# Optimization experiments

Measured on AMD Instinct MI355X. Metric: run time of the kernel, lower is better.

Reference implementation:

```python
import jax, jax.numpy as jnp
import numpy as np

WS = 7  # window size
NH = 12  # num heads
EPS = 1e-5


def setup_inputs() -> dict:
    key = jax.random.key(0)
    ks = jax.random.split(key, 12)
    B, H, W, C = 32, 56, 56, 384
    Dff = 4 * C
    s = lambda k, shape, scale=0.02: jax.random.normal(k, shape, dtype=jnp.float32) * scale
    return {
        "x": jax.random.normal(ks[0], (B, H, W, C), dtype=jnp.float32),
        "ln1_g": jnp.ones((C,), jnp.float32), "ln1_b": jnp.zeros((C,), jnp.float32),
        "qkv_w": s(ks[1], (C, 3 * C)), "qkv_b": jnp.zeros((3 * C,), jnp.float32),
        "proj_w": s(ks[2], (C, C)), "proj_b": jnp.zeros((C,), jnp.float32),
        "ln2_g": jnp.ones((C,), jnp.float32), "ln2_b": jnp.zeros((C,), jnp.float32),
        "mlp_w1": s(ks[3], (C, Dff)), "mlp_b1": jnp.zeros((Dff,), jnp.float32),
        "mlp_w2": s(ks[4], (Dff, C)), "mlp_b2": jnp.zeros((C,), jnp.float32),
    }


def _layernorm(x, g, b):
    m = jnp.mean(x, axis=-1, keepdims=True)
    v = jnp.mean(jnp.square(x - m), axis=-1, keepdims=True)
    return (x - m) * jax.lax.rsqrt(v + EPS) * g + b


def reference(x, ln1_g, ln1_b, qkv_w, qkv_b, proj_w, proj_b, ln2_g, ln2_b,
              mlp_w1, mlp_b1, mlp_w2, mlp_b2):
    B, H, W, C = x.shape
    N = WS * WS
    hd = C // NH
    shortcut = x
    xn = _layernorm(x, ln1_g, ln1_b)
    # window partition: [B,H,W,C] -> [B*nW, N, C]
    xw = xn.reshape(B, H // WS, WS, W // WS, WS, C).transpose(0, 1, 3, 2, 4, 5)
    xw = xw.reshape(-1, N, C)
    # attention within each 49-token window
    qkv = (xw @ qkv_w + qkv_b).reshape(-1, N, 3, NH, hd)
    qkv = qkv.transpose(2, 0, 3, 1, 4)  # [3, Bn, h, N, d]
    q, k, v = qkv[0] * (hd ** -0.5), qkv[1], qkv[2]
    attn = jax.nn.softmax(jnp.einsum('bhnd,bhmd->bhnm', q, k), axis=-1)
    out = jnp.einsum('bhnm,bhmd->bhnd', attn, v)  # [Bn, h, N, d]
    out = out.transpose(0, 2, 1, 3).reshape(-1, N, C)
    out = out @ proj_w + proj_b
    # window unpartition
    xa = out.reshape(B, H // WS, W // WS, WS, WS, C).transpose(0, 1, 3, 2, 4, 5)
    xa = xa.reshape(B, H, W, C)
    x = shortcut + xa
    # MLP (dropout inactive at inference); Keras gelu default is exact
    h = jax.nn.gelu(_layernorm(x, ln2_g, ln2_b) @ mlp_w1 + mlp_b1, approximate=False)
    return x + (h @ mlp_w2 + mlp_b2)
```

## Files before the change

kernel.cpp:

```cpp
#include <hip/hip_runtime.h>
#include <hip/hip_bf16.h>
#include <cstdint>

typedef __bf16 bf16;
typedef __bf16 bf16x8 __attribute__((ext_vector_type(8)));
typedef float f32x4 __attribute__((ext_vector_type(4)));
typedef unsigned int u32;
typedef unsigned short u16;

#define DEV static __device__ __forceinline__

DEV float bfbits2f(u32 bits) { return __builtin_bit_cast(float, bits << 16); }
DEV u16 f2bfbits(float f) {
  u32 u = __builtin_bit_cast(u32, f);
  u32 r = (u + 0x7fffu + ((u >> 16) & 1u)) >> 16;
  return (u16)r;
}

__global__ __launch_bounds__(256) void probe_k(const u32* __restrict__ x, u32* __restrict__ flag) {
  __shared__ int cnt[256];
  int t = threadIdx.x;
  int c = 0;
#pragma unroll
  for (int i = 0; i < 4; ++i) {
    u32 u = x[t * 4 + i];
    u32 e = (u >> 7) & 0xFF;
    c += (e >= 110 && e <= 140) ? 1 : 0;
  }
  cnt[t] = c;
  __syncthreads();
  for (int s = 128; s > 0; s >>= 1) {
    if (t < s) cnt[t] += cnt[t + s];
    __syncthreads();
  }
  if (t == 0) flag[0] = (cnt[0] > 512) ? 1u : 0u;
}

__global__ __launch_bounds__(256) void cvt_params_k(const void* p0, const void* p1,
                                                    const void* p2, const void* p3,
                                                    const void* p4, const void* p5,
                                                    const void* p6, const void* p7,
                                                    float* __restrict__ out,
                                                    const u32* __restrict__ flag) {
  int i = blockIdx.x * 256 + threadIdx.x;
  if (i >= 4992) return;
  const int bounds[9] = {0, 1152, 1536, 3072, 3456, 3840, 4224, 4608, 4992};
  const void* ps[8] = {p0, p1, p2, p3, p4, p5, p6, p7};
  int seg = 0;
  while (i >= bounds[seg + 1]) ++seg;
  int off = i - bounds[seg];
  bool isbf = flag[0] != 0;
  out[i] = isbf ? bfbits2f(((const u16*)ps[seg])[off]) : ((const float*)ps[seg])[off];
}

__global__ __launch_bounds__(256) void transpose_k(const void* __restrict__ in,
                                                   u16* __restrict__ out, int R, int Cc,
                                                   const u32* __restrict__ flag) {
  bool isbf = flag[0] != 0;
  __shared__ u16 tile[32][33];
  int bx = blockIdx.x * 32, by = blockIdx.y * 32;
  int tx = threadIdx.x & 31, ty = threadIdx.x >> 5;
#pragma unroll
  for (int i = 0; i < 32; i += 8) {
    size_t idx = (size_t)(by + ty + i) * Cc + bx + tx;
    u16 v = isbf ? ((const u16*)in)[idx] : f2bfbits(((const float*)in)[idx]);
    tile[ty + i][tx] = v;
  }
  __syncthreads();
#pragma unroll
  for (int i = 0; i < 32; i += 8)
    out[(size_t)(bx + ty + i) * R + by + tx] = tile[tx][ty + i];
}

template <int RAWSRC>
__global__ __launch_bounds__(256) void ln_kernel(const void* __restrict__ xv,
                                                 const float* __restrict__ g,
                                                 const float* __restrict__ b,
                                                 u32* __restrict__ out,
                                                 const u32* __restrict__ flag,
                                                 int windowed, int t0) {
  const int t = t0 + blockIdx.x * 4 + (threadIdx.x >> 6);
  const int lane = threadIdx.x & 63;
  const int e0 = lane * 6;
  float f[6];
  if (RAWSRC) {
    if (flag[0] != 0) {
      const u16* xb = (const u16*)xv + (size_t)t * 384 + e0;
#pragma unroll
      for (int j = 0; j < 6; ++j) f[j] = bfbits2f(xb[j]);
    } else {
      const float* xf = (const float*)xv + (size_t)t * 384 + e0;
#pragma unroll
      for (int j = 0; j < 6; ++j) f[j] = xf[j];
    }
  } else {
    const u32* xr = (const u32*)xv + (size_t)t * 192 + lane * 3;
#pragma unroll
    for (int j = 0; j < 3; ++j) {
      u32 u = xr[j];
      f[2 * j] = bfbits2f(u & 0xffff);
      f[2 * j + 1] = bfbits2f(u >> 16);
    }
  }
  float s = 0.f, q = 0.f;
#pragma unroll
  for (int j = 0; j < 6; ++j) { s += f[j]; q += f[j] * f[j]; }
#pragma unroll
  for (int o = 1; o < 64; o <<= 1) { s += __shfl_xor(s, o); q += __shfl_xor(q, o); }
  float mean = s * (1.0f / 384.0f);
  float var = q * (1.0f / 384.0f) - mean * mean;
  float rstd = rsqrtf(var + 1e-5f);
  int orow;
  if (windowed) {
    int bb = t / 3136, rem = t % 3136;
    int hh = rem / 56, ww = rem % 56;
    orow = (bb * 64 + (hh / 7) * 8 + (ww / 7)) * 49 + (hh % 7) * 7 + (ww % 7) - t0;
  } else {
    orow = t - t0;
  }
  u32* orp = out + (size_t)orow * 192 + lane * 3;
#pragma unroll
  for (int j = 0; j < 3; ++j) {
    float ye = (f[2 * j] - mean) * rstd * g[e0 + 2 * j] + b[e0 + 2 * j];
    float yo = (f[2 * j + 1] - mean) * rstd * g[e0 + 2 * j + 1] + b[e0 + 2 * j + 1];
    orp[j] = (u32)f2bfbits(ye) | ((u32)f2bfbits(yo) << 16);
  }
}

template <int MODE>
__global__ __launch_bounds__(256, 4) void gemm128(const bf16* __restrict__ A,
                                                  const bf16* __restrict__ BT,
                                                  void* __restrict__ Cv,
                                                  const float* __restrict__ bias,
                                                  const void* __restrict__ resv,
                                                  const u32* __restrict__ flag,
                                                  int ldA, int ldC, int K, int rowOff,
                                                  int nN) {
  const int nwg = (int)gridDim.x;
  const int bid = (int)blockIdx.x;
  const int q = nwg >> 3, r = nwg & 7;
  const int xcd = bid & 7, lid = bid >> 3;
  const int wg = (xcd < r ? xcd * (q + 1) : r * (q + 1) + (xcd - r) * q) + lid;
  const int tN = wg % nN, tM = wg / nN;

  const int tid = threadIdx.x;
  const int lane = tid & 63, wave = tid >> 6;
  const int wr = wave >> 1, wc = wave & 1;
  const int li = lane & 15, gq = lane >> 4;
  const bool isbf = flag[0] != 0;

  __shared__ bf16 As[128 * 64];
  __shared__ bf16 Bs[128 * 64];

  f32x4 acc[4][4] = {};

  const bf16* aTile = A + (size_t)tM * 128 * ldA;
  const bf16* bTile = BT + (size_t)tN * 128 * K;

  for (int k0 = 0; k0 < K; k0 += 64) {
#pragma unroll
    for (int i = 0; i < 4; ++i) {
      int c = i * 256 + tid;
      int row = c >> 3, col8 = ((c & 7) ^ (row & 7)) << 3;
      __builtin_amdgcn_global_load_lds(
          (const __attribute__((address_space(1))) void*)(aTile + (size_t)row * ldA + k0 + col8),
          (__attribute__((address_space(3))) void*)(As + (size_t)c * 8), 16, 0, 0);
      __builtin_amdgcn_global_load_lds(
          (const __attribute__((address_space(1))) void*)(bTile + (size_t)row * K + k0 + col8),
          (__attribute__((address_space(3))) void*)(Bs + (size_t)c * 8), 16, 0, 0);
    }
    __syncthreads();
#pragma unroll
    for (int ks = 0; ks < 64; ks += 32) {
      bf16x8 af[4], bfr[4];
#pragma unroll
      for (int m = 0; m < 4; ++m) {
        int arow = wr * 64 + m * 16 + li;
        af[m] = *(const bf16x8*)(As + arow * 64 + ((((ks >> 3) + gq) ^ (arow & 7)) << 3));
      }
#pragma unroll
      for (int n = 0; n < 4; ++n) {
        int brow = wc * 64 + n * 16 + li;
        bfr[n] = *(const bf16x8*)(Bs + brow * 64 + ((((ks >> 3) + gq) ^ (brow & 7)) << 3));
      }
#pragma unroll
      for (int m = 0; m < 4; ++m)
#pragma unroll
        for (int n = 0; n < 4; ++n)
          acc[m][n] = __builtin_amdgcn_mfma_f32_16x16x32_bf16(af[m], bfr[n], acc[m][n], 0, 0, 0);
    }
    __syncthreads();
  }

#pragma unroll
  for (int m = 0; m < 4; ++m) {
#pragma unroll
    for (int r2 = 0; r2 < 4; ++r2) {
      int row = tM * 128 + wr * 64 + m * 16 + gq * 4 + r2;
      size_t crow;
      if (MODE == 1) {
        int gg = rowOff + row;
        int win = gg / 49, n = gg % 49;
        int bb = win >> 6, wi = win & 63;
        int hh = (wi >> 3) * 7 + n / 7;
        int ww = (wi & 7) * 7 + n % 7;
        crow = (size_t)(bb * 3136 + hh * 56 + ww);
      } else {
        crow = (size_t)row;
      }
#pragma unroll
      for (int n = 0; n < 4; ++n) {
        int col = tN * 128 + wc * 64 + n * 16 + li;
        size_t idx = crow * (size_t)ldC + col;
        float v = acc[m][n][r2] + bias[col];
        if (MODE == 2) v = 0.5f * v * (1.0f + erff(v * 0.70710678118654752f));
        if (MODE == 1)
          v += isbf ? bfbits2f(((const u16*)resv)[idx]) : ((const float*)resv)[idx];
        if (MODE == 3) v += bfbits2f(((const u16*)resv)[idx]);
        if (MODE == 3) {
          size_t oidx = idx + (size_t)rowOff * 384;
          if (isbf) ((u16*)Cv)[oidx] = f2bfbits(v);
          else ((float*)Cv)[oidx] = v;
        } else {
          ((u16*)Cv)[idx] = f2bfbits(v);
        }
      }
    }
  }
}

__global__ __launch_bounds__(256, 2) void attn_kernel(const bf16* __restrict__ qkv,
                                                      bf16* __restrict__ out) {
  __shared__ bf16 smem[4 * 6912];
  const int wave = threadIdx.x >> 6;
  const int lane = threadIdx.x & 63;
  const int unit = blockIdx.x * 4 + wave;
  const int win = unit / 12, head = unit % 12;
  bf16* P = smem + wave * 6912;
  bf16* VT = P + 64 * 72;

  const size_t base = (size_t)win * 49 * 1152 + head * 32;
  const bf16* Qp = qkv + base;
  const bf16* Kp = qkv + base + 384;
  const bf16* Vp = qkv + base + 768;

  const int gq = lane >> 4, li = lane & 15;

  {
    int d = lane & 31, half = lane >> 5;
#pragma unroll
    for (int i = 0; i < 32; ++i) {
      int m = i * 2 + half;
      bf16 v = (m < 49) ? Vp[(size_t)m * 1152 + d] : (bf16)0.0f;
      VT[d * 72 + m] = v;
    }
  }

  f32x4 s[4][4] = {};
  bf16x8 qf[4], kf[4];
#pragma unroll
  for (int i = 0; i < 4; ++i) {
    int qr = i * 16 + li; if (qr > 48) qr = 48;
    qf[i] = *(const bf16x8*)(Qp + (size_t)qr * 1152 + gq * 8);
    kf[i] = *(const bf16x8*)(Kp + (size_t)qr * 1152 + gq * 8);
  }
#pragma unroll
  for (int i = 0; i < 4; ++i)
#pragma unroll
    for (int j = 0; j < 4; ++j)
      s[i][j] = __builtin_amdgcn_mfma_f32_16x16x32_bf16(qf[i], kf[j], s[i][j], 0, 0, 0);

  __syncthreads();

  const float scale = 0.17677669529663687f;
#pragma unroll
  for (int i = 0; i < 4; ++i) {
#pragma unroll
    for (int r = 0; r < 4; ++r) {
      float v0 = s[i][0][r] * scale, v1 = s[i][1][r] * scale;
      float v2 = s[i][2][r] * scale, v3 = s[i][3][r] * scale;
      if (li >= 1) v3 = -1e30f;
      float mx = fmaxf(fmaxf(v0, v1), fmaxf(v2, v3));
#pragma unroll
      for (int o = 1; o < 16; o <<= 1) mx = fmaxf(mx, __shfl_xor(mx, o));
      v0 = __expf(v0 - mx); v1 = __expf(v1 - mx);
      v2 = __expf(v2 - mx); v3 = __expf(v3 - mx);
      float sum = v0 + v1 + v2 + v3;
#pragma unroll
      for (int o = 1; o < 16; o <<= 1) sum += __shfl_xor(sum, o);
      float inv = 1.0f / sum;
      int n = i * 16 + gq * 4 + r;
      P[n * 72 + li]      = (bf16)(v0 * inv);
      P[n * 72 + 16 + li] = (bf16)(v1 * inv);
      P[n * 72 + 32 + li] = (bf16)(v2 * inv);
      P[n * 72 + 48 + li] = (bf16)(v3 * inv);
    }
  }

  __syncthreads();

  f32x4 o[4][2] = {};
#pragma unroll
  for (int ms = 0; ms < 2; ++ms) {
    bf16x8 pf[4], vf[2];
#pragma unroll
    for (int i = 0; i < 4; ++i)
      pf[i] = *(const bf16x8*)(P + (i * 16 + li) * 72 + ms * 32 + gq * 8);
#pragma unroll
    for (int dt = 0; dt < 2; ++dt)
      vf[dt] = *(const bf16x8*)(VT + (dt * 16 + li) * 72 + ms * 32 + gq * 8);
#pragma unroll
    for (int i = 0; i < 4; ++i)
#pragma unroll
      for (int dt = 0; dt < 2; ++dt)
        o[i][dt] = __builtin_amdgcn_mfma_f32_16x16x32_bf16(pf[i], vf[dt], o[i][dt], 0, 0, 0);
  }

#pragma unroll
  for (int i = 0; i < 4; ++i) {
#pragma unroll
    for (int r = 0; r < 4; ++r) {
      int n = i * 16 + gq * 4 + r;
      if (n < 49) {
#pragma unroll
        for (int dt = 0; dt < 2; ++dt) {
          int d = dt * 16 + li;
          out[((size_t)win * 49 + n) * 384 + head * 32 + d] = (bf16)o[i][dt][r];
        }
      }
    }
  }
}

extern "C" void kernel_launch(void* const* d_in, const int* in_sizes, int n_in,
                              void* d_out, int out_size, void* d_ws, size_t ws_size,
                              hipStream_t stream) {
  const void* x      = d_in[0];
  const void* ln1_g  = d_in[1];
  const void* ln1_b  = d_in[2];
  const void* qkv_w  = d_in[3];
  const void* qkv_b  = d_in[4];
  const void* proj_w = d_in[5];
  const void* proj_b = d_in[6];
  const void* ln2_g  = d_in[7];
  const void* ln2_b  = d_in[8];
  const void* mlp_w1 = d_in[9];
  const void* mlp_b1 = d_in[10];
  const void* mlp_w2 = d_in[11];
  const void* mlp_b2 = d_in[12];

  char* ws = (char*)d_ws;
  u32* flag = (u32*)ws;
  bf16* qkvwT  = (bf16*)(ws + 256);
  bf16* projwT = qkvwT + 1152 * 384;
  bf16* w1T    = projwT + 384 * 384;
  bf16* w2T    = w1T + 1536 * 384;
  float* pF    = (float*)(ws + 3539200);
  float* qkv_bF  = pF;
  float* proj_bF = pF + 1152;
  float* mlp_b1F = pF + 1536;
  float* mlp_b2F = pF + 3072;
  float* ln1gF   = pF + 3456;
  float* ln1bF   = pF + 3840;
  float* ln2gF   = pF + 4224;
  float* ln2bF   = pF + 4608;
  bf16* x2 = (bf16*)(ws + 3559168);
  char* basep = ws + 80629504ULL;
  const size_t avail = (ws_size > 80629504ULL) ? (ws_size - 80629504ULL) : 0;

  int Wc = 128;
  { const int cand[5] = {2048, 1024, 512, 256, 128};
    for (int i = 0; i < 5; ++i)
      if ((size_t)cand[i] * 49 * 1536 * 2 <= avail) { Wc = cand[i]; break; } }
  int Rc = 6272;
  { const int cand[5] = {100352, 50176, 25088, 12544, 6272};
    for (int i = 0; i < 5; ++i)
      if ((size_t)cand[i] * 1920 * 2 <= avail) { Rc = cand[i]; break; } }

  probe_k<<<1, 256, 0, stream>>>((const u32*)x, flag);

  cvt_params_k<<<20, 256, 0, stream>>>(qkv_b, proj_b, mlp_b1, mlp_b2,
                                       ln1_g, ln1_b, ln2_g, ln2_b, pF, flag);
  transpose_k<<<dim3(36, 12), 256, 0, stream>>>(qkv_w, (u16*)qkvwT, 384, 1152, flag);
  transpose_k<<<dim3(12, 12), 256, 0, stream>>>(proj_w, (u16*)projwT, 384, 384, flag);
  transpose_k<<<dim3(48, 12), 256, 0, stream>>>(mlp_w1, (u16*)w1T, 384, 1536, flag);
  transpose_k<<<dim3(12, 48), 256, 0, stream>>>(mlp_w2, (u16*)w2T, 1536, 384, flag);

  for (int c = 0; c < 2048 / Wc; ++c) {
    const int w0 = c * Wc, t0 = w0 * 49, M = Wc * 49;
    const int nM = M / 128;
    bf16* xn   = (bf16*)basep;
    bf16* qkvb = xn + (size_t)M * 384;
    ln_kernel<1><<<M / 4, 256, 0, stream>>>(x, ln1gF, ln1bF, (u32*)xn, flag, 1, t0);
    gemm128<0><<<dim3(9 * nM), 256, 0, stream>>>(xn, qkvwT, qkvb, qkv_bF, nullptr, flag,
                                                 384, 1152, 384, 0, 9);
    attn_kernel<<<Wc * 3, 256, 0, stream>>>(qkvb, xn);
    gemm128<1><<<dim3(3 * nM), 256, 0, stream>>>(xn, projwT, x2, proj_bF, x, flag,
                                                 384, 384, 384, t0, 3);
  }

  for (int c = 0; c < 100352 / Rc; ++c) {
    const int r0 = c * Rc;
    const int nM = Rc / 128;
    bf16* xn2 = (bf16*)basep;
    bf16* hb  = xn2 + (size_t)Rc * 384;
    ln_kernel<0><<<Rc / 4, 256, 0, stream>>>(x2, ln2gF, ln2bF, (u32*)xn2, flag, 0, r0);
    gemm128<2><<<dim3(12 * nM), 256, 0, stream>>>(xn2, w1T, hb, mlp_b1F, nullptr, flag,
                                                  384, 1536, 384, 0, 12);
    gemm128<3><<<dim3(3 * nM), 256, 0, stream>>>(hb, w2T, d_out, mlp_b2F,
                                                 x2 + (size_t)r0 * 384, flag,
                                                 1536, 384, 1536, r0, 3);
  }
}
```

Measured before the change: 893.8 us.

## Restructure GEMM to 64-row tiles with full-K A in LDS and B in registers

Replaces the 128x128 double-LDS GEMM with a 64x128 tile kernel. The whole 384-wide K chunk of A goes into LDS with a single sync, and each wave keeps its B fragments in registers, loaded straight from global memory. The aim is to remove the per-64-K synchronisation and the LDS traffic for B, and to double the number of M tiles for better occupancy. In exchange, B fragments are reloaded for every M tile, register pressure is high (24 bf16x8 values), and LDS use grows to 48KB, so the occupancy hint drops to 3.

```diff
diff --git a/kernel.cpp b/kernel.cpp
--- a/kernel.cpp
+++ b/kernel.cpp
@@ -128,14 +128,14 @@
 }
 
 template <int MODE>
-__global__ __launch_bounds__(256, 4) void gemm128(const bf16* __restrict__ A,
-                                                  const bf16* __restrict__ BT,
-                                                  void* __restrict__ Cv,
-                                                  const float* __restrict__ bias,
-                                                  const void* __restrict__ resv,
-                                                  const u32* __restrict__ flag,
-                                                  int ldA, int ldC, int K, int rowOff,
-                                                  int nN) {
+__global__ __launch_bounds__(256, 3) void gemm64(const bf16* __restrict__ A,
+                                                 const bf16* __restrict__ BT,
+                                                 void* __restrict__ Cv,
+                                                 const float* __restrict__ bias,
+                                                 const void* __restrict__ resv,
+                                                 const u32* __restrict__ flag,
+                                                 int ldA, int ldC, int K, int rowOff,
+                                                 int nN) {
   const int nwg = (int)gridDim.x;
   const int bid = (int)blockIdx.x;
   const int q = nwg >> 3, r = nwg & 7;
@@ -145,58 +145,60 @@
 
   const int tid = threadIdx.x;
   const int lane = tid & 63, wave = tid >> 6;
-  const int wr = wave >> 1, wc = wave & 1;
   const int li = lane & 15, gq = lane >> 4;
   const bool isbf = flag[0] != 0;
 
-  __shared__ bf16 As[128 * 64];
-  __shared__ bf16 Bs[128 * 64];
-
-  f32x4 acc[4][4] = {};
-
-  const bf16* aTile = A + (size_t)tM * 128 * ldA;
-  const bf16* bTile = BT + (size_t)tN * 128 * K;
-
-  for (int k0 = 0; k0 < K; k0 += 64) {
-#pragma unroll
-    for (int i = 0; i < 4; ++i) {
-      int c = i * 256 + tid;
-      int row = c >> 3, col8 = ((c & 7) ^ (row & 7)) << 3;
+  __shared__ bf16 As[64 * 384];
+
+  f32x4 acc[4][2] = {};
+
+  const bf16* aTile = A + (size_t)tM * 64 * ldA;
+  const int colbase = tN * 128 + wave * 32;
+
+  for (int kc = 0; kc < K; kc += 384) {
+    if (kc) __syncthreads();
+
+    bf16x8 breg[12][2];
+#pragma unroll
+    for (int ks = 0; ks < 12; ++ks)
+#pragma unroll
+      for (int n = 0; n < 2; ++n)
+        breg[ks][n] = *(const bf16x8*)(BT + (size_t)(colbase + n * 16 + li) * K + kc + ks * 32 + gq * 8);
+
+#pragma unroll
+    for (int it = 0; it < 12; ++it) {
+      int c = it * 256 + tid;
+      int row = c / 48, g = c % 48;
+      int gs = (g & ~7) | ((g & 7) ^ (row & 7));
       __builtin_amdgcn_global_load_lds(
-          (const __attribute__((address_space(1))) void*)(aTile + (size_t)row * ldA + k0 + col8),
+          (const __attribute__((address_space(1))) void*)(aTile + (size_t)row * ldA + kc + gs * 8),
           (__attribute__((address_space(3))) void*)(As + (size_t)c * 8), 16, 0, 0);
-      __builtin_amdgcn_global_load_lds(
-          (const __attribute__((address_space(1))) void*)(bTile + (size_t)row * K + k0 + col8),
-          (__attribute__((address_space(3))) void*)(Bs + (size_t)c * 8), 16, 0, 0);
     }
     __syncthreads();
-#pragma unroll
-    for (int ks = 0; ks < 64; ks += 32) {
-      bf16x8 af[4], bfr[4];
+
+#pragma unroll
+    for (int ks = 0; ks < 12; ++ks) {
+      bf16x8 af[4];
 #pragma unroll
       for (int m = 0; m < 4; ++m) {
-        int arow = wr * 64 + m * 16 + li;
-        af[m] = *(const bf16x8*)(As + arow * 64 + ((((ks >> 3) + gq) ^ (arow & 7)) << 3));
+        int arow = m * 16 + li;
+        int g0 = ks * 4 + gq;
+        int gs = (g0 & ~7) | ((g0 & 7) ^ (arow & 7));
+        af[m] = *(const bf16x8*)(As + (size_t)arow * 384 + gs * 8);
       }
 #pragma unroll
-      for (int n = 0; n < 4; ++n) {
-        int brow = wc * 64 + n * 16 + li;
-        bfr[n] = *(const bf16x8*)(Bs + brow * 64 + ((((ks >> 3) + gq) ^ (brow & 7)) << 3));
-      }
-#pragma unroll
       for (int m = 0; m < 4; ++m)
 #pragma unroll
-        for (int n = 0; n < 4; ++n)
-          acc[m][n] = __builtin_amdgcn_mfma_f32_16x16x32_bf16(af[m], bfr[n], acc[m][n], 0, 0, 0);
-    }
-    __syncthreads();
+        for (int n = 0; n < 2; ++n)
+          acc[m][n] = __builtin_amdgcn_mfma_f32_16x16x32_bf16(af[m], breg[ks][n], acc[m][n], 0, 0, 0);
+    }
   }
 
 #pragma unroll
   for (int m = 0; m < 4; ++m) {
 #pragma unroll
     for (int r2 = 0; r2 < 4; ++r2) {
-      int row = tM * 128 + wr * 64 + m * 16 + gq * 4 + r2;
+      int row = tM * 64 + m * 16 + gq * 4 + r2;
       size_t crow;
       if (MODE == 1) {
         int gg = rowOff + row;
@@ -209,8 +211,8 @@
         crow = (size_t)row;
       }
 #pragma unroll
-      for (int n = 0; n < 4; ++n) {
-        int col = tN * 128 + wc * 64 + n * 16 + li;
+      for (int n = 0; n < 2; ++n) {
+        int col = colbase + n * 16 + li;
         size_t idx = crow * (size_t)ldC + col;
         float v = acc[m][n][r2] + bias[col];
         if (MODE == 2) v = 0.5f * v * (1.0f + erff(v * 0.70710678118654752f));
@@ -388,27 +390,27 @@
 
   for (int c = 0; c < 2048 / Wc; ++c) {
     const int w0 = c * Wc, t0 = w0 * 49, M = Wc * 49;
-    const int nM = M / 128;
+    const int nM = M / 64;
     bf16* xn   = (bf16*)basep;
     bf16* qkvb = xn + (size_t)M * 384;
     ln_kernel<1><<<M / 4, 256, 0, stream>>>(x, ln1gF, ln1bF, (u32*)xn, flag, 1, t0);
-    gemm128<0><<<dim3(9 * nM), 256, 0, stream>>>(xn, qkvwT, qkvb, qkv_bF, nullptr, flag,
-                                                 384, 1152, 384, 0, 9);
+    gemm64<0><<<dim3(9 * nM), 256, 0, stream>>>(xn, qkvwT, qkvb, qkv_bF, nullptr, flag,
+                                                384, 1152, 384, 0, 9);
     attn_kernel<<<Wc * 3, 256, 0, stream>>>(qkvb, xn);
-    gemm128<1><<<dim3(3 * nM), 256, 0, stream>>>(xn, projwT, x2, proj_bF, x, flag,
-                                                 384, 384, 384, t0, 3);
+    gemm64<1><<<dim3(3 * nM), 256, 0, stream>>>(xn, projwT, x2, proj_bF, x, flag,
+                                                384, 384, 384, t0, 3);
   }
 
   for (int c = 0; c < 100352 / Rc; ++c) {
     const int r0 = c * Rc;
-    const int nM = Rc / 128;
+    const int nM = Rc / 64;
     bf16* xn2 = (bf16*)basep;
     bf16* hb  = xn2 + (size_t)Rc * 384;
     ln_kernel<0><<<Rc / 4, 256, 0, stream>>>(x2, ln2gF, ln2bF, (u32*)xn2, flag, 0, r0);
-    gemm128<2><<<dim3(12 * nM), 256, 0, stream>>>(xn2, w1T, hb, mlp_b1F, nullptr, flag,
-                                                  384, 1536, 384, 0, 12);
-    gemm128<3><<<dim3(3 * nM), 256, 0, stream>>>(hb, w2T, d_out, mlp_b2F,
-                                                 x2 + (size_t)r0 * 384, flag,
-                                                 1536, 384, 1536, r0, 3);
-  }
-}
+    gemm64<2><<<dim3(12 * nM), 256, 0, stream>>>(xn2, w1T, hb, mlp_b1F, nullptr, flag,
+                                                 384, 1536, 384, 0, 12);
+    gemm64<3><<<dim3(3 * nM), 256, 0, stream>>>(hb, w2T, d_out, mlp_b2F,
+                                                x2 + (size_t)r0 * 384, flag,
+                                                1536, 384, 1536, r0, 3);
+  }
+}
```

After: 1.381 ms. 54.5% more time.

## Double-buffer LDS tiles in GEMM to overlap global loads with MFMA

Applied to the files above, without the earlier changes.

The bf16 GEMM kernel now keeps two LDS buffers for the A and B tiles. It issues the direct-to-LDS loads for the next K-step before computing on the current one, and uses a partial vmcnt wait so the prefetch stays in flight. This aims to hide global memory latency behind the MFMA work instead of stalling on every K-step. LDS use doubles to 64KB per block, so launch bounds drop from 4 to 2 blocks per CU, which lowers occupancy.

```diff
diff --git a/kernel.cpp b/kernel.cpp
--- a/kernel.cpp
+++ b/kernel.cpp
@@ -128,7 +128,7 @@
 }
 
 template <int MODE>
-__global__ __launch_bounds__(256, 4) void gemm128(const bf16* __restrict__ A,
+__global__ __launch_bounds__(256, 2) void gemm128(const bf16* __restrict__ A,
                                                   const bf16* __restrict__ BT,
                                                   void* __restrict__ Cv,
                                                   const float* __restrict__ bias,
@@ -149,39 +149,53 @@
   const int li = lane & 15, gq = lane >> 4;
   const bool isbf = flag[0] != 0;
 
-  __shared__ bf16 As[128 * 64];
-  __shared__ bf16 Bs[128 * 64];
+  __shared__ bf16 As[2][128 * 64];
+  __shared__ bf16 Bs[2][128 * 64];
 
   f32x4 acc[4][4] = {};
 
   const bf16* aTile = A + (size_t)tM * 128 * ldA;
   const bf16* bTile = BT + (size_t)tN * 128 * K;
 
-  for (int k0 = 0; k0 < K; k0 += 64) {
+  auto stage = [&](int buf, int kk) {
 #pragma unroll
     for (int i = 0; i < 4; ++i) {
       int c = i * 256 + tid;
       int row = c >> 3, col8 = ((c & 7) ^ (row & 7)) << 3;
       __builtin_amdgcn_global_load_lds(
-          (const __attribute__((address_space(1))) void*)(aTile + (size_t)row * ldA + k0 + col8),
-          (__attribute__((address_space(3))) void*)(As + (size_t)c * 8), 16, 0, 0);
+          (const __attribute__((address_space(1))) void*)(aTile + (size_t)row * ldA + kk + col8),
+          (__attribute__((address_space(3))) void*)(As[buf] + (size_t)c * 8), 16, 0, 0);
       __builtin_amdgcn_global_load_lds(
-          (const __attribute__((address_space(1))) void*)(bTile + (size_t)row * K + k0 + col8),
-          (__attribute__((address_space(3))) void*)(Bs + (size_t)c * 8), 16, 0, 0);
-    }
-    __syncthreads();
+          (const __attribute__((address_space(1))) void*)(bTile + (size_t)row * K + kk + col8),
+          (__attribute__((address_space(3))) void*)(Bs[buf] + (size_t)c * 8), 16, 0, 0);
+    }
+  };
+
+  const int nt = K >> 6;
+  stage(0, 0);
+  for (int t = 0; t < nt; ++t) {
+    const int cur = t & 1;
+    if (t + 1 < nt) {
+      stage(cur ^ 1, (t + 1) << 6);
+      asm volatile("s_waitcnt vmcnt(8)" ::: "memory");
+    } else {
+      asm volatile("s_waitcnt vmcnt(0)" ::: "memory");
+    }
+    __builtin_amdgcn_sched_barrier(0);
+    __builtin_amdgcn_s_barrier();
+    __builtin_amdgcn_sched_barrier(0);
 #pragma unroll
     for (int ks = 0; ks < 64; ks += 32) {
       bf16x8 af[4], bfr[4];
 #pragma unroll
       for (int m = 0; m < 4; ++m) {
         int arow = wr * 64 + m * 16 + li;
-        af[m] = *(const bf16x8*)(As + arow * 64 + ((((ks >> 3) + gq) ^ (arow & 7)) << 3));
+        af[m] = *(const bf16x8*)(As[cur] + arow * 64 + ((((ks >> 3) + gq) ^ (arow & 7)) << 3));
       }
 #pragma unroll
       for (int n = 0; n < 4; ++n) {
         int brow = wc * 64 + n * 16 + li;
-        bfr[n] = *(const bf16x8*)(Bs + brow * 64 + ((((ks >> 3) + gq) ^ (brow & 7)) << 3));
+        bfr[n] = *(const bf16x8*)(Bs[cur] + brow * 64 + ((((ks >> 3) + gq) ^ (brow & 7)) << 3));
       }
 #pragma unroll
       for (int m = 0; m < 4; ++m)
@@ -189,7 +203,9 @@
         for (int n = 0; n < 4; ++n)
           acc[m][n] = __builtin_amdgcn_mfma_f32_16x16x32_bf16(af[m], bfr[n], acc[m][n], 0, 0, 0);
     }
-    __syncthreads();
+    __builtin_amdgcn_sched_barrier(0);
+    __builtin_amdgcn_s_barrier();
+    __builtin_amdgcn_sched_barrier(0);
   }
 
 #pragma unroll
```

After: 1.076 ms. +20.4%, slower.

## Fold LayerNorm2 into the MLP1 GEMM via per-row stats and weight rescaling

Applied to the files above, without the earlier changes.

LN2 is no longer materialized. Its gamma is folded into the transposed W1, and a per-column vector u plus a beta-folded bias are precomputed. Per-row mean and rstd are computed by a small stats kernel, and the GEMM epilogue applies rstd*acc - rstd*mean*u + bias. This removes the normalized-activation write and reread per chunk, but it multiplies raw x2 (rather than centered values) in bf16 and uses the E[x^2]-mean^2 variance form, which can lose precision.

```diff
diff --git a/kernel.cpp b/kernel.cpp
--- a/kernel.cpp
+++ b/kernel.cpp
@@ -55,7 +55,8 @@
 
 __global__ __launch_bounds__(256) void transpose_k(const void* __restrict__ in,
                                                    u16* __restrict__ out, int R, int Cc,
-                                                   const u32* __restrict__ flag) {
+                                                   const u32* __restrict__ flag,
+                                                   const float* __restrict__ scale) {
   bool isbf = flag[0] != 0;
   __shared__ u16 tile[32][33];
   int bx = blockIdx.x * 32, by = blockIdx.y * 32;
@@ -63,13 +64,59 @@
 #pragma unroll
   for (int i = 0; i < 32; i += 8) {
     size_t idx = (size_t)(by + ty + i) * Cc + bx + tx;
-    u16 v = isbf ? ((const u16*)in)[idx] : f2bfbits(((const float*)in)[idx]);
-    tile[ty + i][tx] = v;
+    float fv = isbf ? bfbits2f(((const u16*)in)[idx]) : ((const float*)in)[idx];
+    if (scale) fv *= scale[by + ty + i];
+    tile[ty + i][tx] = f2bfbits(fv);
   }
   __syncthreads();
 #pragma unroll
   for (int i = 0; i < 32; i += 8)
     out[(size_t)(bx + ty + i) * R + by + tx] = tile[tx][ty + i];
+}
+
+__global__ __launch_bounds__(256) void stats_k(const u32* __restrict__ x2,
+                                               float2* __restrict__ stats) {
+  const int t = blockIdx.x * 4 + (threadIdx.x >> 6);
+  const int lane = threadIdx.x & 63;
+  const u32* xr = x2 + (size_t)t * 192 + lane * 3;
+  float s = 0.f, q = 0.f;
+#pragma unroll
+  for (int j = 0; j < 3; ++j) {
+    u32 u = xr[j];
+    float a = bfbits2f(u & 0xffff), b = bfbits2f(u >> 16);
+    s += a + b;
+    q += a * a + b * b;
+  }
+#pragma unroll
+  for (int o = 1; o < 64; o <<= 1) { s += __shfl_xor(s, o); q += __shfl_xor(q, o); }
+  float mean = s * (1.0f / 384.0f);
+  float var = q * (1.0f / 384.0f) - mean * mean;
+  float rstd = rsqrtf(var + 1e-5f);
+  if (lane == 0) stats[t] = make_float2(rstd, -rstd * mean);
+}
+
+__global__ __launch_bounds__(256) void uv_k(const bf16* __restrict__ w1t,
+                                            const void* __restrict__ w1raw,
+                                            const float* __restrict__ b2,
+                                            const float* __restrict__ b1,
+                                            float* __restrict__ u, float* __restrict__ vb,
+                                            const u32* __restrict__ flag) {
+  const int j = blockIdx.x * 4 + (threadIdx.x >> 6);
+  const int lane = threadIdx.x & 63;
+  const bool isbf = flag[0] != 0;
+  float su = 0.f, sv = 0.f;
+  const bf16* wrow = w1t + (size_t)j * 384;
+#pragma unroll
+  for (int t = 0; t < 6; ++t) {
+    int k = lane * 6 + t;
+    su += (float)wrow[k];
+    float wkj = isbf ? bfbits2f(((const u16*)w1raw)[(size_t)k * 1536 + j])
+                     : ((const float*)w1raw)[(size_t)k * 1536 + j];
+    sv += b2[k] * wkj;
+  }
+#pragma unroll
+  for (int o = 1; o < 64; o <<= 1) { su += __shfl_xor(su, o); sv += __shfl_xor(sv, o); }
+  if (lane == 0) { u[j] = su; vb[j] = sv + b1[j]; }
 }
 
 template <int RAWSRC>
@@ -134,6 +181,8 @@
                                                   const float* __restrict__ bias,
                                                   const void* __restrict__ resv,
                                                   const u32* __restrict__ flag,
+                                                  const float* __restrict__ uvec,
+                                                  const float2* __restrict__ stats,
                                                   int ldA, int ldC, int K, int rowOff,
                                                   int nN) {
   const int nwg = (int)gridDim.x;
@@ -212,8 +261,14 @@
       for (int n = 0; n < 4; ++n) {
         int col = tN * 128 + wc * 64 + n * 16 + li;
         size_t idx = crow * (size_t)ldC + col;
-        float v = acc[m][n][r2] + bias[col];
-        if (MODE == 2) v = 0.5f * v * (1.0f + erff(v * 0.70710678118654752f));
+        float v;
+        if (MODE == 2) {
+          float2 st = stats[rowOff + row];
+          v = st.x * acc[m][n][r2] + st.y * uvec[col] + bias[col];
+          v = 0.5f * v * (1.0f + erff(v * 0.70710678118654752f));
+        } else {
+          v = acc[m][n][r2] + bias[col];
+        }
         if (MODE == 1)
           v += isbf ? bfbits2f(((const u16*)resv)[idx]) : ((const float*)resv)[idx];
         if (MODE == 3) v += bfbits2f(((const u16*)resv)[idx]);
@@ -364,9 +419,12 @@
   float* ln1bF   = pF + 3840;
   float* ln2gF   = pF + 4224;
   float* ln2bF   = pF + 4608;
-  bf16* x2 = (bf16*)(ws + 3559168);
-  char* basep = ws + 80629504ULL;
-  const size_t avail = (ws_size > 80629504ULL) ? (ws_size - 80629504ULL) : 0;
+  float* uvec    = (float*)(ws + 3559168);
+  float* vbvec   = (float*)(ws + 3565312);
+  float2* stats  = (float2*)(ws + 3571456);
+  bf16* x2 = (bf16*)(ws + 4374272);
+  char* basep = ws + 81444608ULL;
+  const size_t avail = (ws_size > 81444608ULL) ? (ws_size - 81444608ULL) : 0;
 
   int Wc = 128;
   { const int cand[5] = {2048, 1024, 512, 256, 128};
@@ -381,10 +439,11 @@
 
   cvt_params_k<<<20, 256, 0, stream>>>(qkv_b, proj_b, mlp_b1, mlp_b2,
                                        ln1_g, ln1_b, ln2_g, ln2_b, pF, flag);
-  transpose_k<<<dim3(36, 12), 256, 0, stream>>>(qkv_w, (u16*)qkvwT, 384, 1152, flag);
-  transpose_k<<<dim3(12, 12), 256, 0, stream>>>(proj_w, (u16*)projwT, 384, 384, flag);
-  transpose_k<<<dim3(48, 12), 256, 0, stream>>>(mlp_w1, (u16*)w1T, 384, 1536, flag);
-  transpose_k<<<dim3(12, 48), 256, 0, stream>>>(mlp_w2, (u16*)w2T, 1536, 384, flag);
+  transpose_k<<<dim3(36, 12), 256, 0, stream>>>(qkv_w, (u16*)qkvwT, 384, 1152, flag, nullptr);
+  transpose_k<<<dim3(12, 12), 256, 0, stream>>>(proj_w, (u16*)projwT, 384, 384, flag, nullptr);
+  transpose_k<<<dim3(48, 12), 256, 0, stream>>>(mlp_w1, (u16*)w1T, 384, 1536, flag, ln2gF);
+  transpose_k<<<dim3(12, 48), 256, 0, stream>>>(mlp_w2, (u16*)w2T, 1536, 384, flag, nullptr);
+  uv_k<<<384, 256, 0, stream>>>(w1T, mlp_w1, ln2bF, mlp_b1F, uvec, vbvec, flag);
 
   for (int c = 0; c < 2048 / Wc; ++c) {
     const int w0 = c * Wc, t0 = w0 * 49, M = Wc * 49;
@@ -393,22 +452,23 @@
     bf16* qkvb = xn + (size_t)M * 384;
     ln_kernel<1><<<M / 4, 256, 0, stream>>>(x, ln1gF, ln1bF, (u32*)xn, flag, 1, t0);
     gemm128<0><<<dim3(9 * nM), 256, 0, stream>>>(xn, qkvwT, qkvb, qkv_bF, nullptr, flag,
-                                                 384, 1152, 384, 0, 9);
+                                                 nullptr, nullptr, 384, 1152, 384, 0, 9);
     attn_kernel<<<Wc * 3, 256, 0, stream>>>(qkvb, xn);
     gemm128<1><<<dim3(3 * nM), 256, 0, stream>>>(xn, projwT, x2, proj_bF, x, flag,
-                                                 384, 384, 384, t0, 3);
-  }
+                                                 nullptr, nullptr, 384, 384, 384, t0, 3);
+  }
+
+  stats_k<<<25088, 256, 0, stream>>>((const u32*)x2, stats);
 
   for (int c = 0; c < 100352 / Rc; ++c) {
     const int r0 = c * Rc;
     const int nM = Rc / 128;
-    bf16* xn2 = (bf16*)basep;
-    bf16* hb  = xn2 + (size_t)Rc * 384;
-    ln_kernel<0><<<Rc / 4, 256, 0, stream>>>(x2, ln2gF, ln2bF, (u32*)xn2, flag, 0, r0);
-    gemm128<2><<<dim3(12 * nM), 256, 0, stream>>>(xn2, w1T, hb, mlp_b1F, nullptr, flag,
-                                                  384, 1536, 384, 0, 12);
+    bf16* hb = (bf16*)basep;
+    gemm128<2><<<dim3(12 * nM), 256, 0, stream>>>(x2 + (size_t)r0 * 384, w1T, hb, vbvec,
+                                                  nullptr, flag, uvec, stats,
+                                                  384, 1536, 384, r0, 12);
     gemm128<3><<<dim3(3 * nM), 256, 0, stream>>>(hb, w2T, d_out, mlp_b2F,
                                                  x2 + (size_t)r0 * 384, flag,
-                                                 1536, 384, 1536, r0, 3);
-  }
-}
+                                                 nullptr, nullptr, 1536, 384, 1536, r0, 3);
+  }
+}
```

New measurement: 893.7 us. No clear change (-0.0%).
